# Kernel tuning notes

Measured on AMD Instinct MI355X. Metric: run time of the kernel, lower is better.

Reference implementation:

```python
import jax, jax.numpy as jnp
import numpy as np

N, D, K = 262144, 64, 1024


def setup_inputs() -> dict:
    key = jax.random.key(0)
    kx, kc = jax.random.split(key)
    x = jax.random.normal(kx, (N, D), dtype=jnp.float32)
    codebook = jax.random.normal(kc, (K, D), dtype=jnp.float32)
    return {"x": x, "codebook": codebook}


def reference(x, codebook):
    # VQTokenizer.encode: cdist(x, codebook) -> argmin -> gather.
    # squared distances equals argmin over cdist (sqrt is monotone).
    x2 = jnp.sum(x * x, axis=-1, keepdims=True)            # (N, 1)
    c2 = jnp.sum(codebook * codebook, axis=-1)             # (K,)
    d2 = x2 + c2[None, :] - 2.0 * jnp.einsum('nd,kd->nk', x, codebook)  # (N, K)
    encoded = jnp.argmin(d2, axis=1)                       # (N,) int
    quantized = jnp.take(codebook, encoded, axis=0)        # (N, D)
    return encoded, quantized
```

## Files before the change

kernel.cpp:

```cpp
#include <hip/hip_runtime.h>
#include <hip/hip_bf16.h>

#define NPTS 262144
#define DDIM 64
#define KCB  1024
#define CHUNK 64
#define NCHUNK (KCB / CHUNK)
#define GPC (CHUNK / 16)
#define PPB 256

typedef __attribute__((ext_vector_type(8))) short short8;
typedef __attribute__((ext_vector_type(4))) float f32x4;

static __device__ __forceinline__ unsigned short f2bf_rne(float f) {
    union { float f; unsigned u; } v; v.f = f;
    unsigned r = v.u + 0x7FFFu + ((v.u >> 16) & 1u);
    return (unsigned short)(r >> 16);
}
static __device__ __forceinline__ float bf2f(unsigned short h) {
    union { unsigned u; float f; } v; v.u = ((unsigned)h) << 16;
    return v.f;
}
static __device__ __forceinline__ bool beats(float sa, int ka, float sb, int kb) {
    return (sa > sb) || (sa == sb && ka < kb);
}
static __device__ __forceinline__ float keyf(float acc, unsigned inv) {
    return __uint_as_float((__float_as_uint(acc) & 0xFFFFFFC0u) | inv);
}

__global__ __launch_bounds__(256) void c2n_kernel(const float* __restrict__ cb,
                                                  float* __restrict__ c2n) {
    int k = blockIdx.x * blockDim.x + threadIdx.x;
    if (k >= KCB) return;
    const float4* row = (const float4*)(cb + (size_t)k * DDIM);
    float s0 = 0.f, s1 = 0.f, s2 = 0.f, s3 = 0.f;
#pragma unroll
    for (int j = 0; j < DDIM / 4; ++j) {
        float4 a = row[j];
        s0 = __builtin_fmaf(a.x, a.x, s0);
        s1 = __builtin_fmaf(a.y, a.y, s1);
        s2 = __builtin_fmaf(a.z, a.z, s2);
        s3 = __builtin_fmaf(a.w, a.w, s3);
    }
    c2n[k] = 256.0f - 0.5f * ((s0 + s1) + (s2 + s3));
}

__global__ __launch_bounds__(256) void pack_kernel(const float* __restrict__ cb,
                                                   unsigned short* __restrict__ G) {
    int t = blockIdx.x * 256 + threadIdx.x;
    int r = t >> 3, d8 = t & 7;
    const float4* src = (const float4*)(cb + (size_t)r * DDIM + d8 * 8);
    float4 v0 = src[0], v1 = src[1];
    float vv[8] = {v0.x, v0.y, v0.z, v0.w, v1.x, v1.y, v1.z, v1.w};
    short8 h, l;
#pragma unroll
    for (int j = 0; j < 8; ++j) {
        unsigned short hb = f2bf_rne(vv[j]);
        h[j] = (short)hb;
        l[j] = (short)f2bf_rne(vv[j] - bf2f(hb));
    }
    int c = r >> 6, g = (r >> 4) & 3, col = r & 15;
    int ks = d8 >> 2, q = d8 & 3;
    size_t base = (size_t)c * 8192 + g * 1024 + ks * 512 + q * 128 + col * 8;
    *(short8*)(G + base) = h;
    *(short8*)(G + base + 4096) = l;
}

__global__ __launch_bounds__(512, 4) void vq_main(const float* __restrict__ x,
                                                  const float* __restrict__ cb,
                                                  const float* __restrict__ c2n,
                                                  const unsigned short* __restrict__ G,
                                                  float* __restrict__ out) {
    __shared__ unsigned short frag[2][CHUNK * DDIM * 2];
    __shared__ int lds_bk1[PPB];
    __shared__ int lds_bk2[PPB];

    const int tid = threadIdx.x;
    const int lane = tid & 63;
    const int wave = tid >> 6;
    const int b15 = lane & 15;
    const int q = lane >> 4;
    const int blk_base = blockIdx.x * PPB;
    const int wave_base = blk_base + wave * 32;
    const int lane_off = lane * 16;

    short8 Ahi[2][2], Alo[2][2];
#pragma unroll
    for (int t = 0; t < 2; ++t) {
        const float* xr = x + (size_t)(wave_base + t * 16 + b15) * DDIM + q * 8;
#pragma unroll
        for (int ks = 0; ks < 2; ++ks) {
            float4 v0 = *(const float4*)(xr + ks * 32);
            float4 v1 = *(const float4*)(xr + ks * 32 + 4);
            float vv[8] = {v0.x, v0.y, v0.z, v0.w, v1.x, v1.y, v1.z, v1.w};
            short8 h, l;
#pragma unroll
            for (int j = 0; j < 8; ++j) {
                unsigned short hb = f2bf_rne(vv[j]);
                h[j] = (short)hb;
                l[j] = (short)f2bf_rne(vv[j] - bf2f(hb));
            }
            Ahi[t][ks] = h;
            Alo[t][ks] = l;
        }
    }

    float b1[8], b2[8];
#pragma unroll
    for (int i = 0; i < 8; ++i) { b1[i] = 0.0f; b2[i] = 0.0f; }

#define STAGE(cc, buf)                                                                     \
    {                                                                                      \
        const unsigned char* gsrc = (const unsigned char*)G + (size_t)(cc) * 16384 + tid * 16; \
        unsigned char* ldst = (unsigned char*)&frag[buf][0] + tid * 16;                    \
        _Pragma("unroll") for (int it = 0; it < 2; ++it)                                   \
            __builtin_amdgcn_global_load_lds(                                              \
                (const __attribute__((address_space(1))) unsigned int*)(gsrc + it * 8192), \
                (__attribute__((address_space(3))) unsigned int*)(ldst + it * 8192),       \
                16, 0, 0);                                                                 \
    }

    float c2v[GPC], c2vn[GPC];
    STAGE(0, 0);
#pragma unroll
    for (int g = 0; g < GPC; ++g) c2v[g] = c2n[g * 16 + b15];
    __syncthreads();

    for (int c = 0; c < NCHUNK; ++c) {
        const int cur = c & 1;
        if (c + 1 < NCHUNK) {
            STAGE(c + 1, cur ^ 1);
#pragma unroll
            for (int g = 0; g < GPC; ++g) c2vn[g] = c2n[(c + 1) * CHUNK + g * 16 + b15];
        }
        const unsigned char* fb = (const unsigned char*)&frag[cur][0];

#pragma unroll
        for (int gp = 0; gp < 2; ++gp) {
            const int g0 = gp * 2, g1 = g0 + 1;
            const unsigned inv0 = 63u - (unsigned)(c * GPC + g0);

            f32x4 acc0[2];
#pragma unroll
            for (int t = 0; t < 2; ++t) acc0[t] = (f32x4){c2v[g0], c2v[g0], c2v[g0], c2v[g0]};
            __builtin_amdgcn_s_setprio(1);
#pragma unroll
            for (int ks = 0; ks < 2; ++ks) {
                const short8 Bhi = *(const short8*)(fb + g0 * 2048 + ks * 1024 + lane_off);
                const short8 Blo = *(const short8*)(fb + 8192 + g0 * 2048 + ks * 1024 + lane_off);
#pragma unroll
                for (int t = 0; t < 2; ++t) {
                    acc0[t] = __builtin_amdgcn_mfma_f32_16x16x32_bf16(Ahi[t][ks], Bhi, acc0[t], 0, 0, 0);
                    acc0[t] = __builtin_amdgcn_mfma_f32_16x16x32_bf16(Ahi[t][ks], Blo, acc0[t], 0, 0, 0);
                    acc0[t] = __builtin_amdgcn_mfma_f32_16x16x32_bf16(Alo[t][ks], Bhi, acc0[t], 0, 0, 0);
                }
            }
            __builtin_amdgcn_s_setprio(0);
            float ka[8];
#pragma unroll
            for (int t = 0; t < 2; ++t)
#pragma unroll
                for (int r = 0; r < 4; ++r) ka[t * 4 + r] = keyf(acc0[t][r], inv0);

            f32x4 acc1[2];
#pragma unroll
            for (int t = 0; t < 2; ++t) acc1[t] = (f32x4){c2v[g1], c2v[g1], c2v[g1], c2v[g1]};
            __builtin_amdgcn_s_setprio(1);
#pragma unroll
            for (int ks = 0; ks < 2; ++ks) {
                const short8 Bhi = *(const short8*)(fb + g1 * 2048 + ks * 1024 + lane_off);
                const short8 Blo = *(const short8*)(fb + 8192 + g1 * 2048 + ks * 1024 + lane_off);
#pragma unroll
                for (int t = 0; t < 2; ++t) {
                    acc1[t] = __builtin_amdgcn_mfma_f32_16x16x32_bf16(Ahi[t][ks], Bhi, acc1[t], 0, 0, 0);
                    acc1[t] = __builtin_amdgcn_mfma_f32_16x16x32_bf16(Ahi[t][ks], Blo, acc1[t], 0, 0, 0);
                    acc1[t] = __builtin_amdgcn_mfma_f32_16x16x32_bf16(Alo[t][ks], Bhi, acc1[t], 0, 0, 0);
                }
            }
            __builtin_amdgcn_s_setprio(0);
#pragma unroll
            for (int t = 0; t < 2; ++t)
#pragma unroll
                for (int r = 0; r < 4; ++r) {
                    const int i = t * 4 + r;
                    const float kb = keyf(acc1[t][r], inv0 - 1u);
                    const float med = __builtin_amdgcn_fmed3f(b1[i], ka[i], kb);
                    float nb1;
                    asm("v_max3_f32 %0, %1, %2, %3" : "=v"(nb1) : "v"(b1[i]), "v"(ka[i]), "v"(kb));
                    b1[i] = nb1;
                    b2[i] = fmaxf(b2[i], med);
                }
        }
#pragma unroll
        for (int g = 0; g < GPC; ++g) c2v[g] = c2vn[g];
        __syncthreads();
    }
#undef STAGE

    unsigned int K1[8], K2[8];
    int I1[8], I2[8];
#pragma unroll
    for (int i = 0; i < 8; ++i) {
        K1[i] = __float_as_uint(b1[i]); I1[i] = (int)(63u - (K1[i] & 63u)) * 16 + b15;
        K2[i] = __float_as_uint(b2[i]); I2[i] = (int)(63u - (K2[i] & 63u)) * 16 + b15;
    }
#pragma unroll
    for (int m = 1; m < 16; m <<= 1) {
#pragma unroll
        for (int i = 0; i < 8; ++i) {
            unsigned int o1 = __shfl_xor(K1[i], m); int oi1 = __shfl_xor(I1[i], m);
            unsigned int o2 = __shfl_xor(K2[i], m); int oi2 = __shfl_xor(I2[i], m);
            bool ob = (o1 > K1[i]) || (o1 == K1[i] && oi1 < I1[i]);
            unsigned int nk1, nk2; int ni1, ni2;
            if (ob) {
                nk1 = o1; ni1 = oi1;
                bool sb = (K1[i] > o2) || (K1[i] == o2 && I1[i] < oi2);
                nk2 = sb ? K1[i] : o2; ni2 = sb ? I1[i] : oi2;
            } else {
                nk1 = K1[i]; ni1 = I1[i];
                bool sb = (o1 > K2[i]) || (o1 == K2[i] && oi1 < I2[i]);
                nk2 = sb ? o1 : K2[i]; ni2 = sb ? oi1 : I2[i];
            }
            K1[i] = nk1; I1[i] = ni1; K2[i] = nk2; I2[i] = ni2;
        }
    }

    if (b15 == 0) {
#pragma unroll
        for (int t = 0; t < 2; ++t)
#pragma unroll
            for (int r = 0; r < 4; ++r) {
                int pl = wave * 32 + t * 16 + q * 4 + r;
                lds_bk1[pl] = I1[t * 4 + r];
                lds_bk2[pl] = I2[t * 4 + r];
            }
    }
    __syncthreads();

    const int pid = tid >> 1;
    const int p = blk_base + pid;
    const int ksel = (tid & 1) ? lds_bk2[pid] : lds_bk1[pid];
    const float4* xr = (const float4*)(x + (size_t)p * DDIM);
    const float4* cr = (const float4*)(cb + (size_t)ksel * DDIM);
    float da = 0.f, db = 0.f;
#pragma unroll
    for (int j = 0; j < 16; ++j) {
        float4 xv = xr[j];
        float4 u = cr[j];
        da = __builtin_fmaf(xv.x, u.x, da); db = __builtin_fmaf(xv.y, u.y, db);
        da = __builtin_fmaf(xv.z, u.z, da); db = __builtin_fmaf(xv.w, u.w, db);
    }
    float a = (da + db) + c2n[ksel];
    float oa = __shfl_xor(a, 1);
    int ok = __shfl_xor(ksel, 1);
    const bool first = ((tid & 1) == 0);
    float a1 = first ? a : oa; int k1 = first ? ksel : ok;
    float a2 = first ? oa : a; int k2 = first ? ok : ksel;
    int kf = beats(a1, k1, a2, k2) ? k1 : k2;

    if (first) out[p] = (float)kf;
    const float4* cf = (const float4*)(cb + (size_t)kf * DDIM + (tid & 1) * 32);
    float4* qo = (float4*)(out + NPTS + (size_t)p * DDIM + (tid & 1) * 32);
#pragma unroll
    for (int j = 0; j < 8; ++j) qo[j] = cf[j];
}

extern "C" void kernel_launch(void* const* d_in, const int* in_sizes, int n_in,
                              void* d_out, int out_size, void* d_ws, size_t ws_size,
                              hipStream_t stream) {
    const float* x = (const float*)d_in[0];
    const float* cb = (const float*)d_in[1];
    float* c2n = (float*)d_ws;
    unsigned short* G = (unsigned short*)((char*)d_ws + 4096);

    hipLaunchKernelGGL(c2n_kernel, dim3(KCB / 256), dim3(256), 0, stream, cb, c2n);
    hipLaunchKernelGGL(pack_kernel, dim3(KCB * 8 / 256), dim3(256), 0, stream, cb, G);
    hipLaunchKernelGGL(vq_main, dim3(NPTS / PPB), dim3(512), 0, stream,
                       x, cb, c2n, G, (float*)d_out);
}
```

Measured before the change: 142.0 us.

## Load codebook fragments directly from global into registers, dropping LDS staging

The codebook fragment layout is repacked per 16-column group so each lane can read its MFMA B operands straight from global memory (L2/L1-cached) with register double-buffering, instead of staging 64-row chunks into shared memory through global_load_lds and synchronising with barriers. This removes the per-chunk __syncthreads and the shared-memory footprint. In exchange, every wave issues its own global loads for the whole codebook, which adds cache traffic and exposes global latency that only one group of prefetch can hide.

```diff
diff --git a/kernel.cpp b/kernel.cpp
--- a/kernel.cpp
+++ b/kernel.cpp
@@ -4,9 +4,7 @@
 #define NPTS 262144
 #define DDIM 64
 #define KCB  1024
-#define CHUNK 64
-#define NCHUNK (KCB / CHUNK)
-#define GPC (CHUNK / 16)
+#define NGRP (KCB / 16)
 #define PPB 256
 
 typedef __attribute__((ext_vector_type(8))) short short8;
@@ -59,19 +57,20 @@
         h[j] = (short)hb;
         l[j] = (short)f2bf_rne(vv[j] - bf2f(hb));
     }
-    int c = r >> 6, g = (r >> 4) & 3, col = r & 15;
+    int g = r >> 4, col = r & 15;
     int ks = d8 >> 2, q = d8 & 3;
-    size_t base = (size_t)c * 8192 + g * 1024 + ks * 512 + q * 128 + col * 8;
+    size_t base = (size_t)g * 2048 + ks * 1024 + q * 128 + col * 8;
     *(short8*)(G + base) = h;
-    *(short8*)(G + base + 4096) = l;
-}
+    *(short8*)(G + base + 512) = l;
+}
+
+struct BFrag { short8 h0, l0, h1, l1; };
 
 __global__ __launch_bounds__(512, 4) void vq_main(const float* __restrict__ x,
                                                   const float* __restrict__ cb,
                                                   const float* __restrict__ c2n,
                                                   const unsigned short* __restrict__ G,
                                                   float* __restrict__ out) {
-    __shared__ unsigned short frag[2][CHUNK * DDIM * 2];
     __shared__ int lds_bk1[PPB];
     __shared__ int lds_bk2[PPB];
 
@@ -82,7 +81,7 @@
     const int q = lane >> 4;
     const int blk_base = blockIdx.x * PPB;
     const int wave_base = blk_base + wave * 32;
-    const int lane_off = lane * 16;
+    const unsigned char* Gb = (const unsigned char*)G + lane * 16;
 
     short8 Ahi[2][2], Alo[2][2];
 #pragma unroll
@@ -109,93 +108,70 @@
 #pragma unroll
     for (int i = 0; i < 8; ++i) { b1[i] = 0.0f; b2[i] = 0.0f; }
 
-#define STAGE(cc, buf)                                                                     \
-    {                                                                                      \
-        const unsigned char* gsrc = (const unsigned char*)G + (size_t)(cc) * 16384 + tid * 16; \
-        unsigned char* ldst = (unsigned char*)&frag[buf][0] + tid * 16;                    \
-        _Pragma("unroll") for (int it = 0; it < 2; ++it)                                   \
-            __builtin_amdgcn_global_load_lds(                                              \
-                (const __attribute__((address_space(1))) unsigned int*)(gsrc + it * 8192), \
-                (__attribute__((address_space(3))) unsigned int*)(ldst + it * 8192),       \
-                16, 0, 0);                                                                 \
-    }
-
-    float c2v[GPC], c2vn[GPC];
-    STAGE(0, 0);
-#pragma unroll
-    for (int g = 0; g < GPC; ++g) c2v[g] = c2n[g * 16 + b15];
-    __syncthreads();
-
-    for (int c = 0; c < NCHUNK; ++c) {
-        const int cur = c & 1;
-        if (c + 1 < NCHUNK) {
-            STAGE(c + 1, cur ^ 1);
-#pragma unroll
-            for (int g = 0; g < GPC; ++g) c2vn[g] = c2n[(c + 1) * CHUNK + g * 16 + b15];
-        }
-        const unsigned char* fb = (const unsigned char*)&frag[cur][0];
-
-#pragma unroll
-        for (int gp = 0; gp < 2; ++gp) {
-            const int g0 = gp * 2, g1 = g0 + 1;
-            const unsigned inv0 = 63u - (unsigned)(c * GPC + g0);
-
-            f32x4 acc0[2];
-#pragma unroll
-            for (int t = 0; t < 2; ++t) acc0[t] = (f32x4){c2v[g0], c2v[g0], c2v[g0], c2v[g0]};
-            __builtin_amdgcn_s_setprio(1);
-#pragma unroll
-            for (int ks = 0; ks < 2; ++ks) {
-                const short8 Bhi = *(const short8*)(fb + g0 * 2048 + ks * 1024 + lane_off);
-                const short8 Blo = *(const short8*)(fb + 8192 + g0 * 2048 + ks * 1024 + lane_off);
-#pragma unroll
-                for (int t = 0; t < 2; ++t) {
-                    acc0[t] = __builtin_amdgcn_mfma_f32_16x16x32_bf16(Ahi[t][ks], Bhi, acc0[t], 0, 0, 0);
-                    acc0[t] = __builtin_amdgcn_mfma_f32_16x16x32_bf16(Ahi[t][ks], Blo, acc0[t], 0, 0, 0);
-                    acc0[t] = __builtin_amdgcn_mfma_f32_16x16x32_bf16(Alo[t][ks], Bhi, acc0[t], 0, 0, 0);
-                }
-            }
-            __builtin_amdgcn_s_setprio(0);
-            float ka[8];
-#pragma unroll
-            for (int t = 0; t < 2; ++t)
-#pragma unroll
-                for (int r = 0; r < 4; ++r) ka[t * 4 + r] = keyf(acc0[t][r], inv0);
-
-            f32x4 acc1[2];
-#pragma unroll
-            for (int t = 0; t < 2; ++t) acc1[t] = (f32x4){c2v[g1], c2v[g1], c2v[g1], c2v[g1]};
-            __builtin_amdgcn_s_setprio(1);
-#pragma unroll
-            for (int ks = 0; ks < 2; ++ks) {
-                const short8 Bhi = *(const short8*)(fb + g1 * 2048 + ks * 1024 + lane_off);
-                const short8 Blo = *(const short8*)(fb + 8192 + g1 * 2048 + ks * 1024 + lane_off);
-#pragma unroll
-                for (int t = 0; t < 2; ++t) {
-                    acc1[t] = __builtin_amdgcn_mfma_f32_16x16x32_bf16(Ahi[t][ks], Bhi, acc1[t], 0, 0, 0);
-                    acc1[t] = __builtin_amdgcn_mfma_f32_16x16x32_bf16(Ahi[t][ks], Blo, acc1[t], 0, 0, 0);
-                    acc1[t] = __builtin_amdgcn_mfma_f32_16x16x32_bf16(Alo[t][ks], Bhi, acc1[t], 0, 0, 0);
-                }
-            }
-            __builtin_amdgcn_s_setprio(0);
-#pragma unroll
-            for (int t = 0; t < 2; ++t)
-#pragma unroll
-                for (int r = 0; r < 4; ++r) {
-                    const int i = t * 4 + r;
-                    const float kb = keyf(acc1[t][r], inv0 - 1u);
-                    const float med = __builtin_amdgcn_fmed3f(b1[i], ka[i], kb);
-                    float nb1;
-                    asm("v_max3_f32 %0, %1, %2, %3" : "=v"(nb1) : "v"(b1[i]), "v"(ka[i]), "v"(kb));
-                    b1[i] = nb1;
-                    b2[i] = fmaxf(b2[i], med);
-                }
-        }
-#pragma unroll
-        for (int g = 0; g < GPC; ++g) c2v[g] = c2vn[g];
-        __syncthreads();
-    }
-#undef STAGE
+#define LOADB(dst, g)                                                   \
+    {                                                                   \
+        const unsigned char* gb_ = Gb + (size_t)(g) * 4096;             \
+        (dst).h0 = *(const short8*)(gb_);                               \
+        (dst).l0 = *(const short8*)(gb_ + 1024);                        \
+        (dst).h1 = *(const short8*)(gb_ + 2048);                        \
+        (dst).l1 = *(const short8*)(gb_ + 3072);                        \
+    }
+#define COMPUTE(acc, B, c2vx)                                                                   \
+    {                                                                                           \
+        _Pragma("unroll") for (int t = 0; t < 2; ++t)                                           \
+            acc[t] = (f32x4){c2vx, c2vx, c2vx, c2vx};                                           \
+        __builtin_amdgcn_s_setprio(1);                                                          \
+        _Pragma("unroll") for (int t = 0; t < 2; ++t) {                                         \
+            acc[t] = __builtin_amdgcn_mfma_f32_16x16x32_bf16(Ahi[t][0], (B).h0, acc[t], 0, 0, 0); \
+            acc[t] = __builtin_amdgcn_mfma_f32_16x16x32_bf16(Ahi[t][0], (B).l0, acc[t], 0, 0, 0); \
+            acc[t] = __builtin_amdgcn_mfma_f32_16x16x32_bf16(Alo[t][0], (B).h0, acc[t], 0, 0, 0); \
+            acc[t] = __builtin_amdgcn_mfma_f32_16x16x32_bf16(Ahi[t][1], (B).h1, acc[t], 0, 0, 0); \
+            acc[t] = __builtin_amdgcn_mfma_f32_16x16x32_bf16(Ahi[t][1], (B).l1, acc[t], 0, 0, 0); \
+            acc[t] = __builtin_amdgcn_mfma_f32_16x16x32_bf16(Alo[t][1], (B).h1, acc[t], 0, 0, 0); \
+        }                                                                                       \
+        __builtin_amdgcn_s_setprio(0);                                                          \
+    }
+
+    BFrag Ba, Bb;
+    LOADB(Ba, 0);
+    float c2v0 = c2n[b15], c2v1 = c2n[16 + b15];
+
+    for (int gp = 0; gp < 32; ++gp) {
+        const int g0 = gp * 2;
+        const unsigned inv0 = 63u - (unsigned)g0;
+        LOADB(Bb, g0 + 1);
+        float n0 = c2n[((g0 + 2) & 63) * 16 + b15];
+        float n1 = c2n[((g0 + 3) & 63) * 16 + b15];
+
+        f32x4 acc0[2];
+        COMPUTE(acc0, Ba, c2v0);
+        float ka[8];
+#pragma unroll
+        for (int t = 0; t < 2; ++t)
+#pragma unroll
+            for (int r = 0; r < 4; ++r) ka[t * 4 + r] = keyf(acc0[t][r], inv0);
+
+        LOADB(Ba, (g0 + 2) & 63);
+
+        f32x4 acc1[2];
+        COMPUTE(acc1, Bb, c2v1);
+#pragma unroll
+        for (int t = 0; t < 2; ++t)
+#pragma unroll
+            for (int r = 0; r < 4; ++r) {
+                const int i = t * 4 + r;
+                const float kb = keyf(acc1[t][r], inv0 - 1u);
+                const float med = __builtin_amdgcn_fmed3f(b1[i], ka[i], kb);
+                float nb1;
+                asm("v_max3_f32 %0, %1, %2, %3" : "=v"(nb1) : "v"(b1[i]), "v"(ka[i]), "v"(kb));
+                b1[i] = nb1;
+                b2[i] = fmaxf(b2[i], med);
+            }
+        c2v0 = n0;
+        c2v1 = n1;
+    }
+#undef LOADB
+#undef COMPUTE
 
     unsigned int K1[8], K2[8];
     int I1[8], I2[8];
```

Measured after the change: 150.9 us. 1.06x slower.

## Double codebook chunk size, stage c2 norms in LDS, batch B fragment loads

Applied to the files above, without the earlier changes.

Raises the per-iteration codebook chunk from 64 to 128 entries, with matching changes to the pack layout and staging size. This halves the number of chunk iterations and __syncthreads barriers. The c2 norms are preloaded once into LDS instead of being prefetched per chunk from global memory. The LDS B fragments for two groups are also loaded together before the MFMA chains. In exchange, the kernel uses twice the LDS per block for the double buffer, which could cut the number of resident blocks per CU at 4 blocks of 512 threads. It also adds register pressure from holding two B fragment sets at once.

```diff
diff --git a/kernel.cpp b/kernel.cpp
--- a/kernel.cpp
+++ b/kernel.cpp
@@ -4,7 +4,7 @@
 #define NPTS 262144
 #define DDIM 64
 #define KCB  1024
-#define CHUNK 64
+#define CHUNK 128
 #define NCHUNK (KCB / CHUNK)
 #define GPC (CHUNK / 16)
 #define PPB 256
@@ -59,12 +59,14 @@
         h[j] = (short)hb;
         l[j] = (short)f2bf_rne(vv[j] - bf2f(hb));
     }
-    int c = r >> 6, g = (r >> 4) & 3, col = r & 15;
+    int c = r >> 7, g = (r >> 4) & 7, col = r & 15;
     int ks = d8 >> 2, q = d8 & 3;
-    size_t base = (size_t)c * 8192 + g * 1024 + ks * 512 + q * 128 + col * 8;
+    size_t base = (size_t)c * 16384 + g * 1024 + ks * 512 + q * 128 + col * 8;
     *(short8*)(G + base) = h;
-    *(short8*)(G + base + 4096) = l;
-}
+    *(short8*)(G + base + 8192) = l;
+}
+
+struct BFrag { short8 h0, l0, h1, l1; };
 
 __global__ __launch_bounds__(512, 4) void vq_main(const float* __restrict__ x,
                                                   const float* __restrict__ cb,
@@ -72,6 +74,7 @@
                                                   const unsigned short* __restrict__ G,
                                                   float* __restrict__ out) {
     __shared__ unsigned short frag[2][CHUNK * DDIM * 2];
+    __shared__ float lds_c2f[KCB];
     __shared__ int lds_bk1[PPB];
     __shared__ int lds_bk2[PPB];
 
@@ -111,91 +114,83 @@
 
 #define STAGE(cc, buf)                                                                     \
     {                                                                                      \
-        const unsigned char* gsrc = (const unsigned char*)G + (size_t)(cc) * 16384 + tid * 16; \
+        const unsigned char* gsrc = (const unsigned char*)G + (size_t)(cc) * 32768 + tid * 16; \
         unsigned char* ldst = (unsigned char*)&frag[buf][0] + tid * 16;                    \
-        _Pragma("unroll") for (int it = 0; it < 2; ++it)                                   \
+        _Pragma("unroll") for (int it = 0; it < 4; ++it)                                   \
             __builtin_amdgcn_global_load_lds(                                              \
                 (const __attribute__((address_space(1))) unsigned int*)(gsrc + it * 8192), \
                 (__attribute__((address_space(3))) unsigned int*)(ldst + it * 8192),       \
                 16, 0, 0);                                                                 \
     }
-
-    float c2v[GPC], c2vn[GPC];
+#define LOADB(dst, fb, g)                                               \
+    {                                                                   \
+        const unsigned char* p_ = (fb) + (size_t)(g) * 2048 + lane_off; \
+        (dst).h0 = *(const short8*)(p_);                                \
+        (dst).l0 = *(const short8*)(p_ + 16384);                        \
+        (dst).h1 = *(const short8*)(p_ + 1024);                         \
+        (dst).l1 = *(const short8*)(p_ + 17408);                        \
+    }
+#define COMPUTE(acc, B, cvec)                                                                    \
+    {                                                                                            \
+        __builtin_amdgcn_s_setprio(1);                                                           \
+        _Pragma("unroll") for (int t = 0; t < 2; ++t) {                                          \
+            acc[t] = __builtin_amdgcn_mfma_f32_16x16x32_bf16(Ahi[t][0], (B).h0, cvec, 0, 0, 0);  \
+            acc[t] = __builtin_amdgcn_mfma_f32_16x16x32_bf16(Ahi[t][0], (B).l0, acc[t], 0, 0, 0);\
+            acc[t] = __builtin_amdgcn_mfma_f32_16x16x32_bf16(Alo[t][0], (B).h0, acc[t], 0, 0, 0);\
+            acc[t] = __builtin_amdgcn_mfma_f32_16x16x32_bf16(Ahi[t][1], (B).h1, acc[t], 0, 0, 0);\
+            acc[t] = __builtin_amdgcn_mfma_f32_16x16x32_bf16(Ahi[t][1], (B).l1, acc[t], 0, 0, 0);\
+            acc[t] = __builtin_amdgcn_mfma_f32_16x16x32_bf16(Alo[t][1], (B).h1, acc[t], 0, 0, 0);\
+        }                                                                                        \
+        __builtin_amdgcn_s_setprio(0);                                                           \
+    }
+
     STAGE(0, 0);
-#pragma unroll
-    for (int g = 0; g < GPC; ++g) c2v[g] = c2n[g * 16 + b15];
+    lds_c2f[tid] = c2n[tid];
+    lds_c2f[tid + 512] = c2n[tid + 512];
     __syncthreads();
 
     for (int c = 0; c < NCHUNK; ++c) {
         const int cur = c & 1;
-        if (c + 1 < NCHUNK) {
-            STAGE(c + 1, cur ^ 1);
-#pragma unroll
-            for (int g = 0; g < GPC; ++g) c2vn[g] = c2n[(c + 1) * CHUNK + g * 16 + b15];
-        }
+        if (c + 1 < NCHUNK) STAGE(c + 1, cur ^ 1);
         const unsigned char* fb = (const unsigned char*)&frag[cur][0];
 
 #pragma unroll
-        for (int gp = 0; gp < 2; ++gp) {
+        for (int gp = 0; gp < 4; ++gp) {
             const int g0 = gp * 2, g1 = g0 + 1;
             const unsigned inv0 = 63u - (unsigned)(c * GPC + g0);
+            BFrag Ba, Bb;
+            LOADB(Ba, fb, g0);
+            LOADB(Bb, fb, g1);
+            const float cg0 = lds_c2f[(c * GPC + g0) * 16 + b15];
+            const float cg1 = lds_c2f[(c * GPC + g1) * 16 + b15];
 
             f32x4 acc0[2];
-#pragma unroll
-            for (int t = 0; t < 2; ++t) acc0[t] = (f32x4){c2v[g0], c2v[g0], c2v[g0], c2v[g0]};
-            __builtin_amdgcn_s_setprio(1);
-#pragma unroll
-            for (int ks = 0; ks < 2; ++ks) {
-                const short8 Bhi = *(const short8*)(fb + g0 * 2048 + ks * 1024 + lane_off);
-                const short8 Blo = *(const short8*)(fb + 8192 + g0 * 2048 + ks * 1024 + lane_off);
-#pragma unroll
-                for (int t = 0; t < 2; ++t) {
-                    acc0[t] = __builtin_amdgcn_mfma_f32_16x16x32_bf16(Ahi[t][ks], Bhi, acc0[t], 0, 0, 0);
-                    acc0[t] = __builtin_amdgcn_mfma_f32_16x16x32_bf16(Ahi[t][ks], Blo, acc0[t], 0, 0, 0);
-                    acc0[t] = __builtin_amdgcn_mfma_f32_16x16x32_bf16(Alo[t][ks], Bhi, acc0[t], 0, 0, 0);
-                }
-            }
-            __builtin_amdgcn_s_setprio(0);
-            float ka[8];
-#pragma unroll
-            for (int t = 0; t < 2; ++t)
-#pragma unroll
-                for (int r = 0; r < 4; ++r) ka[t * 4 + r] = keyf(acc0[t][r], inv0);
-
+            const f32x4 cvec0 = (f32x4){cg0, cg0, cg0, cg0};
+            COMPUTE(acc0, Ba, cvec0);
             f32x4 acc1[2];
-#pragma unroll
-            for (int t = 0; t < 2; ++t) acc1[t] = (f32x4){c2v[g1], c2v[g1], c2v[g1], c2v[g1]};
-            __builtin_amdgcn_s_setprio(1);
-#pragma unroll
-            for (int ks = 0; ks < 2; ++ks) {
-                const short8 Bhi = *(const short8*)(fb + g1 * 2048 + ks * 1024 + lane_off);
-                const short8 Blo = *(const short8*)(fb + 8192 + g1 * 2048 + ks * 1024 + lane_off);
-#pragma unroll
-                for (int t = 0; t < 2; ++t) {
-                    acc1[t] = __builtin_amdgcn_mfma_f32_16x16x32_bf16(Ahi[t][ks], Bhi, acc1[t], 0, 0, 0);
-                    acc1[t] = __builtin_amdgcn_mfma_f32_16x16x32_bf16(Ahi[t][ks], Blo, acc1[t], 0, 0, 0);
-                    acc1[t] = __builtin_amdgcn_mfma_f32_16x16x32_bf16(Alo[t][ks], Bhi, acc1[t], 0, 0, 0);
-                }
-            }
-            __builtin_amdgcn_s_setprio(0);
+            const f32x4 cvec1 = (f32x4){cg1, cg1, cg1, cg1};
+            COMPUTE(acc1, Bb, cvec1);
+
 #pragma unroll
             for (int t = 0; t < 2; ++t)
 #pragma unroll
                 for (int r = 0; r < 4; ++r) {
                     const int i = t * 4 + r;
+                    const float ka = keyf(acc0[t][r], inv0);
                     const float kb = keyf(acc1[t][r], inv0 - 1u);
-                    const float med = __builtin_amdgcn_fmed3f(b1[i], ka[i], kb);
+                    const float med = __builtin_amdgcn_fmed3f(b1[i], ka, kb);
                     float nb1;
-                    asm("v_max3_f32 %0, %1, %2, %3" : "=v"(nb1) : "v"(b1[i]), "v"(ka[i]), "v"(kb));
+                    asm("v_max3_f32 %0, %1, %2, %3"
+                        : "=v"(nb1) : "v"(b1[i]), "v"(ka), "v"(kb));
                     b1[i] = nb1;
                     b2[i] = fmaxf(b2[i], med);
                 }
         }
-#pragma unroll
-        for (int g = 0; g < GPC; ++g) c2v[g] = c2vn[g];
         __syncthreads();
     }
 #undef STAGE
+#undef LOADB
+#undef COMPUTE
 
     unsigned int K1[8], K2[8];
     int I1[8], I2[8];
```

Measured after the change: 138.9 us. -2.2%, faster.

## Shrink codebook chunks and blocks, restructure packed layout and per-group top-2 update

Applied to the files above, without the earlier changes.

Halves the codebook chunk staged into LDS per iteration and the points per block (256-thread blocks, launch bounds raised to 8 blocks per CU). The packed bf16 hi/lo layout is changed so each 16-entry group is contiguous. The inner loop now processes one group at a time, loading all B fragments up front, reading c2n directly per group instead of prefetching, and using a simpler med3/max top-2 update. The aim is higher occupancy and lower register pressure, at the cost of twice as many chunk iterations and barriers plus an extra global load per group. Parts of the hidden code, such as the frag size and the epilogue's use of PPB, must match the new constants.

```diff
diff --git a/kernel.cpp b/kernel.cpp
--- a/kernel.cpp
+++ b/kernel.cpp
@@ -4,10 +4,9 @@
 #define NPTS 262144
 #define DDIM 64
 #define KCB  1024
-#define CHUNK 64
+#define CHUNK 32
 #define NCHUNK (KCB / CHUNK)
-#define GPC (CHUNK / 16)
-#define PPB 256
+#define PPB 128
 
 typedef __attribute__((ext_vector_type(8))) short short8;
 typedef __attribute__((ext_vector_type(4))) float f32x4;
@@ -59,14 +58,16 @@
         h[j] = (short)hb;
         l[j] = (short)f2bf_rne(vv[j] - bf2f(hb));
     }
-    int c = r >> 6, g = (r >> 4) & 3, col = r & 15;
+    int g = r >> 4, col = r & 15;
     int ks = d8 >> 2, q = d8 & 3;
-    size_t base = (size_t)c * 8192 + g * 1024 + ks * 512 + q * 128 + col * 8;
+    size_t base = (size_t)g * 2048 + ks * 512 + q * 128 + col * 8;
     *(short8*)(G + base) = h;
-    *(short8*)(G + base + 4096) = l;
-}
-
-__global__ __launch_bounds__(512, 4) void vq_main(const float* __restrict__ x,
+    *(short8*)(G + base + 1024) = l;
+}
+
+struct BFrag { short8 h0, l0, h1, l1; };
+
+__global__ __launch_bounds__(256, 8) void vq_main(const float* __restrict__ x,
                                                   const float* __restrict__ cb,
                                                   const float* __restrict__ c2n,
                                                   const unsigned short* __restrict__ G,
@@ -111,88 +112,61 @@
 
 #define STAGE(cc, buf)                                                                     \
     {                                                                                      \
-        const unsigned char* gsrc = (const unsigned char*)G + (size_t)(cc) * 16384 + tid * 16; \
+        const unsigned char* gsrc = (const unsigned char*)G + (size_t)(cc) * 8192 + tid * 16; \
         unsigned char* ldst = (unsigned char*)&frag[buf][0] + tid * 16;                    \
         _Pragma("unroll") for (int it = 0; it < 2; ++it)                                   \
             __builtin_amdgcn_global_load_lds(                                              \
-                (const __attribute__((address_space(1))) unsigned int*)(gsrc + it * 8192), \
-                (__attribute__((address_space(3))) unsigned int*)(ldst + it * 8192),       \
+                (const __attribute__((address_space(1))) unsigned int*)(gsrc + it * 4096), \
+                (__attribute__((address_space(3))) unsigned int*)(ldst + it * 4096),       \
                 16, 0, 0);                                                                 \
     }
 
-    float c2v[GPC], c2vn[GPC];
     STAGE(0, 0);
-#pragma unroll
-    for (int g = 0; g < GPC; ++g) c2v[g] = c2n[g * 16 + b15];
     __syncthreads();
 
-    for (int c = 0; c < NCHUNK; ++c) {
-        const int cur = c & 1;
-        if (c + 1 < NCHUNK) {
-            STAGE(c + 1, cur ^ 1);
-#pragma unroll
-            for (int g = 0; g < GPC; ++g) c2vn[g] = c2n[(c + 1) * CHUNK + g * 16 + b15];
-        }
+    for (int cc = 0; cc < NCHUNK; ++cc) {
+        const int cur = cc & 1;
+        if (cc + 1 < NCHUNK) STAGE(cc + 1, cur ^ 1);
         const unsigned char* fb = (const unsigned char*)&frag[cur][0];
 
 #pragma unroll
-        for (int gp = 0; gp < 2; ++gp) {
-            const int g0 = gp * 2, g1 = g0 + 1;
-            const unsigned inv0 = 63u - (unsigned)(c * GPC + g0);
-
-            f32x4 acc0[2];
-#pragma unroll
-            for (int t = 0; t < 2; ++t) acc0[t] = (f32x4){c2v[g0], c2v[g0], c2v[g0], c2v[g0]};
+        for (int gl = 0; gl < 2; ++gl) {
+            const int gg = cc * 2 + gl;
+            const unsigned inv = 63u - (unsigned)gg;
+            BFrag B;
+            {
+                const unsigned char* p_ = fb + gl * 4096 + lane_off;
+                B.h0 = *(const short8*)(p_);
+                B.l0 = *(const short8*)(p_ + 2048);
+                B.h1 = *(const short8*)(p_ + 1024);
+                B.l1 = *(const short8*)(p_ + 3072);
+            }
+            const float cg = c2n[gg * 16 + b15];
+            const f32x4 cvec = (f32x4){cg, cg, cg, cg};
+
+            f32x4 acc[2];
             __builtin_amdgcn_s_setprio(1);
 #pragma unroll
-            for (int ks = 0; ks < 2; ++ks) {
-                const short8 Bhi = *(const short8*)(fb + g0 * 2048 + ks * 1024 + lane_off);
-                const short8 Blo = *(const short8*)(fb + 8192 + g0 * 2048 + ks * 1024 + lane_off);
-#pragma unroll
-                for (int t = 0; t < 2; ++t) {
-                    acc0[t] = __builtin_amdgcn_mfma_f32_16x16x32_bf16(Ahi[t][ks], Bhi, acc0[t], 0, 0, 0);
-                    acc0[t] = __builtin_amdgcn_mfma_f32_16x16x32_bf16(Ahi[t][ks], Blo, acc0[t], 0, 0, 0);
-                    acc0[t] = __builtin_amdgcn_mfma_f32_16x16x32_bf16(Alo[t][ks], Bhi, acc0[t], 0, 0, 0);
-                }
+            for (int t = 0; t < 2; ++t) {
+                acc[t] = __builtin_amdgcn_mfma_f32_16x16x32_bf16(Ahi[t][0], B.h0, cvec, 0, 0, 0);
+                acc[t] = __builtin_amdgcn_mfma_f32_16x16x32_bf16(Ahi[t][0], B.l0, acc[t], 0, 0, 0);
+                acc[t] = __builtin_amdgcn_mfma_f32_16x16x32_bf16(Alo[t][0], B.h0, acc[t], 0, 0, 0);
+                acc[t] = __builtin_amdgcn_mfma_f32_16x16x32_bf16(Ahi[t][1], B.h1, acc[t], 0, 0, 0);
+                acc[t] = __builtin_amdgcn_mfma_f32_16x16x32_bf16(Ahi[t][1], B.l1, acc[t], 0, 0, 0);
+                acc[t] = __builtin_amdgcn_mfma_f32_16x16x32_bf16(Alo[t][1], B.h1, acc[t], 0, 0, 0);
             }
             __builtin_amdgcn_s_setprio(0);
-            float ka[8];
-#pragma unroll
-            for (int t = 0; t < 2; ++t)
-#pragma unroll
-                for (int r = 0; r < 4; ++r) ka[t * 4 + r] = keyf(acc0[t][r], inv0);
-
-            f32x4 acc1[2];
-#pragma unroll
-            for (int t = 0; t < 2; ++t) acc1[t] = (f32x4){c2v[g1], c2v[g1], c2v[g1], c2v[g1]};
-            __builtin_amdgcn_s_setprio(1);
-#pragma unroll
-            for (int ks = 0; ks < 2; ++ks) {
-                const short8 Bhi = *(const short8*)(fb + g1 * 2048 + ks * 1024 + lane_off);
-                const short8 Blo = *(const short8*)(fb + 8192 + g1 * 2048 + ks * 1024 + lane_off);
-#pragma unroll
-                for (int t = 0; t < 2; ++t) {
-                    acc1[t] = __builtin_amdgcn_mfma_f32_16x16x32_bf16(Ahi[t][ks], Bhi, acc1[t], 0, 0, 0);
-                    acc1[t] = __builtin_amdgcn_mfma_f32_16x16x32_bf16(Ahi[t][ks], Blo, acc1[t], 0, 0, 0);
-                    acc1[t] = __builtin_amdgcn_mfma_f32_16x16x32_bf16(Alo[t][ks], Bhi, acc1[t], 0, 0, 0);
-                }
-            }
-            __builtin_amdgcn_s_setprio(0);
+
 #pragma unroll
             for (int t = 0; t < 2; ++t)
 #pragma unroll
                 for (int r = 0; r < 4; ++r) {
                     const int i = t * 4 + r;
-                    const float kb = keyf(acc1[t][r], inv0 - 1u);
-                    const float med = __builtin_amdgcn_fmed3f(b1[i], ka[i], kb);
-                    float nb1;
-                    asm("v_max3_f32 %0, %1, %2, %3" : "=v"(nb1) : "v"(b1[i]), "v"(ka[i]), "v"(kb));
-                    b1[i] = nb1;
-                    b2[i] = fmaxf(b2[i], med);
+                    const float kk = keyf(acc[t][r], inv);
+                    b2[i] = __builtin_amdgcn_fmed3f(kk, b1[i], b2[i]);
+                    b1[i] = fmaxf(b1[i], kk);
                 }
         }
-#pragma unroll
-        for (int g = 0; g < GPC; ++g) c2v[g] = c2vn[g];
         __syncthreads();
     }
 #undef STAGE
@@ -275,6 +249,6 @@
 
     hipLaunchKernelGGL(c2n_kernel, dim3(KCB / 256), dim3(256), 0, stream, cb, c2n);
     hipLaunchKernelGGL(pack_kernel, dim3(KCB * 8 / 256), dim3(256), 0, stream, cb, G);
-    hipLaunchKernelGGL(vq_main, dim3(NPTS / PPB), dim3(512), 0, stream,
+    hipLaunchKernelGGL(vq_main, dim3(NPTS / PPB), dim3(256), 0, stream,
                        x, cb, c2n, G, (float*)d_out);
 }
```

After: 494.5 us. +248.2%, slower.
